# Performance work log

Measured on AMD Instinct MI355X. Metric: run time of the kernel, lower is better.

## Reference

```python
import jax, jax.numpy as jnp
import numpy as np

B, T, DE, NIV, MH, H = 32768, 200, 6, 8, 16, 128  # batch, timesteps, strain dim, internal vars, encoder half-width, hidden
DT = 0.01
DIN = DE + NIV + 2 * MH  # 46: input dim of both tiny MLPs


def setup_inputs() -> dict:
    key = jax.random.key(0)
    ks = jax.random.split(key, 12)

    def glorot(k, shape):
        return jax.random.normal(k, shape, jnp.float32) / np.sqrt(shape[-1])

    return dict(
        e=jax.random.normal(ks[0], (B, T, DE), jnp.float32),
        e_dot=jax.random.normal(ks[1], (B, T, DE), jnp.float32),
        E=jax.random.uniform(ks[2], (B, 1), jnp.float32),
        nu=jax.random.uniform(ks[3], (B, 1), jnp.float32),
        # energy MLP: Linear(DIN,H) -> relu^2 -> Linear(H,2)
        We1=glorot(ks[4], (H, DIN)), be1=jnp.zeros((H,), jnp.float32),
        We2=glorot(ks[5], (2, H)), be2=jnp.zeros((2,), jnp.float32),
        # dissipation MLP: Linear(DIN,H) -> relu^2 -> Linear(H,1)
        Wd1=glorot(ks[6], (H, DIN)), bd1=jnp.zeros((H,), jnp.float32),
        Wd2=glorot(ks[7], (1, H)), bd2=jnp.zeros((1,), jnp.float32),
        # microstructure encoders: Linear(1, MH) each
        WE=glorot(ks[8], (MH, 1)), bE=jnp.zeros((MH,), jnp.float32),
        Wnu=glorot(ks[9], (MH, 1)), bnu=jnp.zeros((MH,), jnp.float32),
    )


def _grad_sq_mlp(u, v, m, W1, b1, W2):
    # d/dx = (2 * relu(h) * sum_rows(W2)) @ W1
    x = jnp.concatenate([u, v, m], axis=-1)  # [B, DIN]
    r = jax.nn.relu(x @ W1.T + b1)           # [B, H]
    return (2.0 * r * W2.sum(0)) @ W1        # [B, DIN]


def _forward(e, e_dot, E, nu, We1, be1, We2, be2, Wd1, bd1, Wd2, bd2, WE, bE, Wnu, bnu):
    m = jnp.concatenate([E @ WE.T + bE, nu @ Wnu.T + bnu], axis=-1)  # [B, 2*MH]
    xi0 = jnp.zeros((e.shape[0], NIV), e.dtype)

    def step(xi, inp):
        et, edt = inp
        ge = _grad_sq_mlp(et, xi, m, We1, be1, We2)      # dPsi/d(e, xi)
        s_eq = ge[:, :DE]
        d = ge[:, DE:DE + NIV]
        gd = _grad_sq_mlp(edt, -d, m, Wd1, bd1, Wd2)     # dPhi/d(e_dot, -d)
        s_neq = gd[:, :DE]
        kinetics = gd[:, DE:DE + NIV]
        return xi + DT * kinetics, (s_eq - s_neq, xi)

    _, (stress, xi) = jax.lax.scan(
        step, xi0, (jnp.swapaxes(e, 0, 1), jnp.swapaxes(e_dot, 0, 1)))
    return jnp.swapaxes(stress, 0, 1), jnp.swapaxes(xi, 0, 1)


def reference(e, e_dot, E, nu, We1, be1, We2, be2, Wd1, bd1, Wd2, bd2, WE, bE, Wnu, bnu):
    return _forward(e, e_dot, E, nu, We1, be1, We2, be2, Wd1, bd1, Wd2, bd2, WE, bE, Wnu, bnu)
```

## Files before the change

kernel.cpp:

```cpp
#include <hip/hip_runtime.h>

#define NB   32768
#define NT   200
#define DE   6
#define NIV  8
#define MH   16
#define NH   128
#define DTC  0.01f

#define LSTR 20

__global__ __launch_bounds__(256, 2)
void visco_fused(const float* __restrict__ e, const float* __restrict__ edot,
                 const float* __restrict__ Ein, const float* __restrict__ nuin,
                 const float* __restrict__ We1, const float* __restrict__ be1,
                 const float* __restrict__ We2,
                 const float* __restrict__ Wd1, const float* __restrict__ bd1,
                 const float* __restrict__ Wd2,
                 const float* __restrict__ WE,  const float* __restrict__ bE,
                 const float* __restrict__ Wnu, const float* __restrict__ bnu,
                 float* __restrict__ out_stress, float* __restrict__ out_xi)
{
    __shared__ float LE[NH * LSTR];
    __shared__ float LD[NH * LSTR];

    const int tid = threadIdx.x;

    if (tid < NH) {
        const int j = tid;
        {
            const float* row = We1 + j * 46;
            float alpha = be1[j], beta = 0.f, gamma = 0.f;
            #pragma unroll
            for (int k = 0; k < MH; ++k) {
                alpha += bE[k]  * row[14 + k] + bnu[k] * row[30 + k];
                beta  += WE[k]  * row[14 + k];
                gamma += Wnu[k] * row[30 + k];
            }
            #pragma unroll
            for (int i = 0; i < 14; ++i) LE[j * LSTR + i] = row[i];
            LE[j * LSTR + 14] = alpha;
            LE[j * LSTR + 15] = beta;
            LE[j * LSTR + 16] = gamma;
            LE[j * LSTR + 17] = 2.0f * (We2[j] + We2[NH + j]);
        }
        {
            const float* row = Wd1 + j * 46;
            float alpha = bd1[j], beta = 0.f, gamma = 0.f;
            #pragma unroll
            for (int k = 0; k < MH; ++k) {
                alpha += bE[k]  * row[14 + k] + bnu[k] * row[30 + k];
                beta  += WE[k]  * row[14 + k];
                gamma += Wnu[k] * row[30 + k];
            }
            #pragma unroll
            for (int i = 0; i < 14; ++i) LD[j * LSTR + i] = row[i];
            LD[j * LSTR + 14] = alpha;
            LD[j * LSTR + 15] = beta;
            LD[j * LSTR + 16] = gamma;
            LD[j * LSTR + 17] = 2.0f * Wd2[j];
        }
    }
    __syncthreads();

    const int gt   = blockIdx.x * 256 + tid;
    const int elem = gt >> 2;
    const int s    = tid & 3;

    const float Ev  = Ein[elem];
    const float nuv = nuin[elem];

    float xi[NIV];
    #pragma unroll
    for (int i = 0; i < NIV; ++i) xi[i] = 0.f;

    const float* ep = e    + (size_t)elem * (NT * DE);
    const float* dp = edot + (size_t)elem * (NT * DE);
    float* sp = out_stress + (size_t)elem * (NT * DE);
    float* xp = out_xi     + (size_t)elem * (NT * NIV);

    float2 ea = *(const float2*)(ep + 0);
    float2 eb = *(const float2*)(ep + 2);
    float2 ec = *(const float2*)(ep + 4);
    float2 da = *(const float2*)(dp + 0);
    float2 db = *(const float2*)(dp + 2);
    float2 dc = *(const float2*)(dp + 4);

    #pragma unroll 1
    for (int t = 0; t < NT; ++t) {
        const int tn = (t + 1 < NT) ? (t + 1) : t;
        float2 na = *(const float2*)(ep + tn * DE + 0);
        float2 nb = *(const float2*)(ep + tn * DE + 2);
        float2 nc = *(const float2*)(ep + tn * DE + 4);
        float2 ma = *(const float2*)(dp + tn * DE + 0);
        float2 mb = *(const float2*)(dp + tn * DE + 2);
        float2 mc = *(const float2*)(dp + tn * DE + 4);

        float g[14];
        #pragma unroll
        for (int i = 0; i < 14; ++i) g[i] = 0.f;

        #pragma unroll 2
        for (int jj = 0; jj < 32; ++jj) {
            const float* row = &LE[(4 * jj + s) * LSTR];
            float h = fmaf(Ev, row[15], row[14]);
            h = fmaf(nuv,  row[16], h);
            h = fmaf(ea.x, row[0],  h);
            h = fmaf(ea.y, row[1],  h);
            h = fmaf(eb.x, row[2],  h);
            h = fmaf(eb.y, row[3],  h);
            h = fmaf(ec.x, row[4],  h);
            h = fmaf(ec.y, row[5],  h);
            h = fmaf(xi[0], row[6],  h);
            h = fmaf(xi[1], row[7],  h);
            h = fmaf(xi[2], row[8],  h);
            h = fmaf(xi[3], row[9],  h);
            h = fmaf(xi[4], row[10], h);
            h = fmaf(xi[5], row[11], h);
            h = fmaf(xi[6], row[12], h);
            h = fmaf(xi[7], row[13], h);
            const float a = fmaxf(h, 0.f) * row[17];
            #pragma unroll
            for (int i = 0; i < 14; ++i) g[i] = fmaf(a, row[i], g[i]);
        }
        #pragma unroll
        for (int i = 0; i < 14; ++i) {
            g[i] += __shfl_xor(g[i], 1);
            g[i] += __shfl_xor(g[i], 2);
        }

        float q[14];
        #pragma unroll
        for (int i = 0; i < 14; ++i) q[i] = 0.f;

        #pragma unroll 2
        for (int jj = 0; jj < 32; ++jj) {
            const float* row = &LD[(4 * jj + s) * LSTR];
            float h = fmaf(Ev, row[15], row[14]);
            h = fmaf(nuv,  row[16], h);
            h = fmaf(da.x, row[0],  h);
            h = fmaf(da.y, row[1],  h);
            h = fmaf(db.x, row[2],  h);
            h = fmaf(db.y, row[3],  h);
            h = fmaf(dc.x, row[4],  h);
            h = fmaf(dc.y, row[5],  h);
            h = fmaf(-g[6],  row[6],  h);
            h = fmaf(-g[7],  row[7],  h);
            h = fmaf(-g[8],  row[8],  h);
            h = fmaf(-g[9],  row[9],  h);
            h = fmaf(-g[10], row[10], h);
            h = fmaf(-g[11], row[11], h);
            h = fmaf(-g[12], row[12], h);
            h = fmaf(-g[13], row[13], h);
            const float a = fmaxf(h, 0.f) * row[17];
            #pragma unroll
            for (int i = 0; i < 14; ++i) q[i] = fmaf(a, row[i], q[i]);
        }
        #pragma unroll
        for (int i = 0; i < 14; ++i) {
            q[i] += __shfl_xor(q[i], 1);
            q[i] += __shfl_xor(q[i], 2);
        }

        if (s == 0) {
            float2* o = (float2*)(sp + t * DE);
            o[0] = make_float2(g[0] - q[0], g[1] - q[1]);
            o[1] = make_float2(g[2] - q[2], g[3] - q[3]);
            o[2] = make_float2(g[4] - q[4], g[5] - q[5]);
        } else if (s == 1) {
            *(float4*)(xp + t * NIV)     = make_float4(xi[0], xi[1], xi[2], xi[3]);
        } else if (s == 2) {
            *(float4*)(xp + t * NIV + 4) = make_float4(xi[4], xi[5], xi[6], xi[7]);
        }

        #pragma unroll
        for (int i = 0; i < NIV; ++i) xi[i] = fmaf(DTC, q[6 + i], xi[i]);

        ea = na; eb = nb; ec = nc;
        da = ma; db = mb; dc = mc;
    }
}

extern "C" void kernel_launch(void* const* d_in, const int* in_sizes, int n_in,
                              void* d_out, int out_size, void* d_ws, size_t ws_size,
                              hipStream_t stream) {
    const float* e    = (const float*)d_in[0];
    const float* edot = (const float*)d_in[1];
    const float* E    = (const float*)d_in[2];
    const float* nu   = (const float*)d_in[3];
    const float* We1  = (const float*)d_in[4];
    const float* be1  = (const float*)d_in[5];
    const float* We2  = (const float*)d_in[6];
    const float* Wd1  = (const float*)d_in[8];
    const float* bd1  = (const float*)d_in[9];
    const float* Wd2  = (const float*)d_in[10];
    const float* WE   = (const float*)d_in[12];
    const float* bE   = (const float*)d_in[13];
    const float* Wnu  = (const float*)d_in[14];
    const float* bnu  = (const float*)d_in[15];

    float* out_stress = (float*)d_out;
    float* out_xi     = out_stress + (size_t)NB * NT * DE;

    const int threads = NB * 4;
    dim3 grid(threads / 256), block(256);
    visco_fused<<<grid, block, 0, stream>>>(e, edot, E, nu, We1, be1, We2,
                                            Wd1, bd1, Wd2, WE, bE, Wnu, bnu,
                                            out_stress, out_xi);
}
```

Baseline: 2.045 ms.

## Split each batch element across 8 lanes and precompute per-element bias terms

Each batch element is now handled by 8 lanes instead of 4. Each lane covers 16 hidden units rather than 32, and an extra shuffle-xor stage completes the reduction. The per-element E/nu bias contribution for every hidden unit is precomputed once into registers (baseE/baseD), which removes two FMAs per unit per timestep. Shared-memory setup now uses all 256 threads, launch bounds ask for 4 blocks per CU, and the grid doubles. The trade-off is more shuffle and reduction work per step and more threads in total, in exchange for more parallelism and a shorter serial chain per timestep.

New measurement: 2.261 ms. +10.5%, slower.

```diff
diff --git a/kernel.cpp b/kernel.cpp
--- a/kernel.cpp
+++ b/kernel.cpp
@@ -10,65 +10,60 @@
 
 #define LSTR 20
 
-__global__ __launch_bounds__(256, 2)
-void visco_fused(const float* __restrict__ e, const float* __restrict__ edot,
-                 const float* __restrict__ Ein, const float* __restrict__ nuin,
-                 const float* __restrict__ We1, const float* __restrict__ be1,
-                 const float* __restrict__ We2,
-                 const float* __restrict__ Wd1, const float* __restrict__ bd1,
-                 const float* __restrict__ Wd2,
-                 const float* __restrict__ WE,  const float* __restrict__ bE,
-                 const float* __restrict__ Wnu, const float* __restrict__ bnu,
-                 float* __restrict__ out_stress, float* __restrict__ out_xi)
+__global__ __launch_bounds__(256, 4)
+void visco_fused8(const float* __restrict__ e, const float* __restrict__ edot,
+                  const float* __restrict__ Ein, const float* __restrict__ nuin,
+                  const float* __restrict__ We1, const float* __restrict__ be1,
+                  const float* __restrict__ We2,
+                  const float* __restrict__ Wd1, const float* __restrict__ bd1,
+                  const float* __restrict__ Wd2,
+                  const float* __restrict__ WE,  const float* __restrict__ bE,
+                  const float* __restrict__ Wnu, const float* __restrict__ bnu,
+                  float* __restrict__ out_stress, float* __restrict__ out_xi)
 {
     __shared__ float LE[NH * LSTR];
     __shared__ float LD[NH * LSTR];
 
     const int tid = threadIdx.x;
 
-    if (tid < NH) {
-        const int j = tid;
-        {
-            const float* row = We1 + j * 46;
-            float alpha = be1[j], beta = 0.f, gamma = 0.f;
-            #pragma unroll
-            for (int k = 0; k < MH; ++k) {
-                alpha += bE[k]  * row[14 + k] + bnu[k] * row[30 + k];
-                beta  += WE[k]  * row[14 + k];
-                gamma += Wnu[k] * row[30 + k];
-            }
-            #pragma unroll
-            for (int i = 0; i < 14; ++i) LE[j * LSTR + i] = row[i];
-            LE[j * LSTR + 14] = alpha;
-            LE[j * LSTR + 15] = beta;
-            LE[j * LSTR + 16] = gamma;
-            LE[j * LSTR + 17] = 2.0f * (We2[j] + We2[NH + j]);
-        }
-        {
-            const float* row = Wd1 + j * 46;
-            float alpha = bd1[j], beta = 0.f, gamma = 0.f;
-            #pragma unroll
-            for (int k = 0; k < MH; ++k) {
-                alpha += bE[k]  * row[14 + k] + bnu[k] * row[30 + k];
-                beta  += WE[k]  * row[14 + k];
-                gamma += Wnu[k] * row[30 + k];
-            }
-            #pragma unroll
-            for (int i = 0; i < 14; ++i) LD[j * LSTR + i] = row[i];
-            LD[j * LSTR + 14] = alpha;
-            LD[j * LSTR + 15] = beta;
-            LD[j * LSTR + 16] = gamma;
-            LD[j * LSTR + 17] = 2.0f * Wd2[j];
-        }
+    {
+        const int j = tid & 127;
+        const float* W1 = (tid < NH) ? We1 : Wd1;
+        const float* b1 = (tid < NH) ? be1 : bd1;
+        float*       L  = (tid < NH) ? LE  : LD;
+        const float* row = W1 + j * 46;
+        float alpha = b1[j], beta = 0.f, gamma = 0.f;
+        #pragma unroll
+        for (int k = 0; k < MH; ++k) {
+            alpha += bE[k]  * row[14 + k] + bnu[k] * row[30 + k];
+            beta  += WE[k]  * row[14 + k];
+            gamma += Wnu[k] * row[30 + k];
+        }
+        #pragma unroll
+        for (int i = 0; i < 14; ++i) L[j * LSTR + i] = row[i];
+        L[j * LSTR + 14] = (tid < NH) ? (2.0f * (We2[j] + We2[NH + j]))
+                                      : (2.0f * Wd2[j]);
+        L[j * LSTR + 15] = alpha;
+        L[j * LSTR + 16] = beta;
+        L[j * LSTR + 17] = gamma;
     }
     __syncthreads();
 
     const int gt   = blockIdx.x * 256 + tid;
-    const int elem = gt >> 2;
-    const int s    = tid & 3;
+    const int elem = gt >> 3;
+    const int s    = tid & 7;
 
     const float Ev  = Ein[elem];
     const float nuv = nuin[elem];
+
+    float baseE[16], baseD[16];
+    #pragma unroll
+    for (int jj = 0; jj < 16; ++jj) {
+        const float* re = &LE[(8 * jj + s) * LSTR];
+        const float* rd = &LD[(8 * jj + s) * LSTR];
+        baseE[jj] = fmaf(nuv, re[17], fmaf(Ev, re[16], re[15]));
+        baseD[jj] = fmaf(nuv, rd[17], fmaf(Ev, rd[16], rd[15]));
+    }
 
     float xi[NIV];
     #pragma unroll
@@ -101,10 +96,9 @@
         for (int i = 0; i < 14; ++i) g[i] = 0.f;
 
         #pragma unroll 2
-        for (int jj = 0; jj < 32; ++jj) {
-            const float* row = &LE[(4 * jj + s) * LSTR];
-            float h = fmaf(Ev, row[15], row[14]);
-            h = fmaf(nuv,  row[16], h);
+        for (int jj = 0; jj < 16; ++jj) {
+            const float* row = &LE[(8 * jj + s) * LSTR];
+            float h = baseE[jj];
             h = fmaf(ea.x, row[0],  h);
             h = fmaf(ea.y, row[1],  h);
             h = fmaf(eb.x, row[2],  h);
@@ -119,7 +113,7 @@
             h = fmaf(xi[5], row[11], h);
             h = fmaf(xi[6], row[12], h);
             h = fmaf(xi[7], row[13], h);
-            const float a = fmaxf(h, 0.f) * row[17];
+            const float a = fmaxf(h, 0.f) * row[14];
             #pragma unroll
             for (int i = 0; i < 14; ++i) g[i] = fmaf(a, row[i], g[i]);
         }
@@ -127,6 +121,7 @@
         for (int i = 0; i < 14; ++i) {
             g[i] += __shfl_xor(g[i], 1);
             g[i] += __shfl_xor(g[i], 2);
+            g[i] += __shfl_xor(g[i], 4);
         }
 
         float q[14];
@@ -134,10 +129,9 @@
         for (int i = 0; i < 14; ++i) q[i] = 0.f;
 
         #pragma unroll 2
-        for (int jj = 0; jj < 32; ++jj) {
-            const float* row = &LD[(4 * jj + s) * LSTR];
-            float h = fmaf(Ev, row[15], row[14]);
-            h = fmaf(nuv,  row[16], h);
+        for (int jj = 0; jj < 16; ++jj) {
+            const float* row = &LD[(8 * jj + s) * LSTR];
+            float h = baseD[jj];
             h = fmaf(da.x, row[0],  h);
             h = fmaf(da.y, row[1],  h);
             h = fmaf(db.x, row[2],  h);
@@ -152,7 +146,7 @@
             h = fmaf(-g[11], row[11], h);
             h = fmaf(-g[12], row[12], h);
             h = fmaf(-g[13], row[13], h);
-            const float a = fmaxf(h, 0.f) * row[17];
+            const float a = fmaxf(h, 0.f) * row[14];
             #pragma unroll
             for (int i = 0; i < 14; ++i) q[i] = fmaf(a, row[i], q[i]);
         }
@@ -160,6 +154,7 @@
         for (int i = 0; i < 14; ++i) {
             q[i] += __shfl_xor(q[i], 1);
             q[i] += __shfl_xor(q[i], 2);
+            q[i] += __shfl_xor(q[i], 4);
         }
 
         if (s == 0) {
@@ -202,9 +197,9 @@
     float* out_stress = (float*)d_out;
     float* out_xi     = out_stress + (size_t)NB * NT * DE;
 
-    const int threads = NB * 4;
+    const int threads = NB * 8;
     dim3 grid(threads / 256), block(256);
-    visco_fused<<<grid, block, 0, stream>>>(e, edot, E, nu, We1, be1, We2,
-                                            Wd1, bd1, Wd2, WE, bE, Wnu, bnu,
-                                            out_stress, out_xi);
+    visco_fused8<<<grid, block, 0, stream>>>(e, edot, E, nu, We1, be1, We2,
+                                             Wd1, bd1, Wd2, WE, bE, Wnu, bnu,
+                                             out_stress, out_xi);
 }
```
